# Performance work log

Measured on AMD Instinct MI355X. Metric: run time of the kernel, lower is better.

Reference implementation:

```python
import jax, jax.numpy as jnp
import numpy as np
import math

D_MODEL = 512
H = 8
N_LAYERS = 4
D_FF = 2048
HEAD_DIM = D_MODEL // H


def setup_inputs() -> dict:
    key = jax.random.key(0)
    ks = jax.random.split(key, 12)
    s = 1.0 / math.sqrt(D_MODEL)
    x = jax.random.normal(ks[0], (16, 1024, D_MODEL), dtype=jnp.float32)
    # shared head module (same weights for all H heads, per original ModuleList aliasing)
    wq = jax.random.normal(ks[1], (D_MODEL, HEAD_DIM), dtype=jnp.float32) * s
    bq = jnp.zeros((HEAD_DIM,), dtype=jnp.float32)
    wk = jax.random.normal(ks[2], (D_MODEL, HEAD_DIM), dtype=jnp.float32) * s
    bk = jnp.zeros((HEAD_DIM,), dtype=jnp.float32)
    wv = jax.random.normal(ks[3], (D_MODEL, HEAD_DIM), dtype=jnp.float32) * s
    bv = jnp.zeros((HEAD_DIM,), dtype=jnp.float32)
    wo = jax.random.normal(ks[4], (D_MODEL, D_MODEL), dtype=jnp.float32) * s
    bo = jnp.zeros((D_MODEL,), dtype=jnp.float32)
    # shared LayerNorm params (one LN instance used everywhere)
    ln_g = jnp.ones((D_MODEL,), dtype=jnp.float32)
    ln_b = jnp.zeros((D_MODEL,), dtype=jnp.float32)
    w1 = jax.random.normal(ks[5], (D_MODEL, D_FF), dtype=jnp.float32) * s
    b1 = jnp.zeros((D_FF,), dtype=jnp.float32)
    w2 = jax.random.normal(ks[6], (D_FF, D_MODEL), dtype=jnp.float32) * (1.0 / math.sqrt(D_FF))
    b2 = jnp.zeros((D_MODEL,), dtype=jnp.float32)
    return {"x": x, "wq": wq, "bq": bq, "wk": wk, "bk": bk, "wv": wv, "bv": bv,
            "wo": wo, "bo": bo, "ln_g": ln_g, "ln_b": ln_b,
            "w1": w1, "b1": b1, "w2": w2, "b2": b2}


def _layernorm(x, g, b, eps=1e-5):
    mu = jnp.mean(x, axis=-1, keepdims=True)
    var = jnp.var(x, axis=-1, keepdims=True)
    return (x - mu) * jax.lax.rsqrt(var + eps) * g + b


def _mha(x, wq, bq, wk, bk, wv, bv, wo, bo):
    # All H heads share identical weights, so compute one head and tile the concat.
    q = x @ wq + bq                      # [b, s, hd]
    k = x @ wk + bk                      # [b, s, hd]
    v = x @ wv + bv                      # [b, s, hd]
    scores = jnp.einsum('bqd,bkd->bqk', q, k) / math.sqrt(D_MODEL / H)
    # NOTE: original applies Softmax(dim=1) on a [b, s_q, s_k] tensor -> softmax over q axis
    attn = jax.nn.softmax(scores, axis=1)
    head = jnp.einsum('bqk,bkd->bqd', attn, v)   # [b, s, hd]
    concat = jnp.tile(head, (1, 1, H))           # [b, s, d_model] (H identical heads)
    return concat @ wo + bo


def reference(x, wq, bq, wk, bk, wv, bv, wo, bo, ln_g, ln_b, w1, b1, w2, b2):
    for _ in range(N_LAYERS):
        attn = _mha(x, wq, bq, wk, bk, wv, bv, wo, bo)
        h = _layernorm(attn + x, ln_g, ln_b)
        ff = (jnp.maximum(h @ w1 + b1, 0.0) if False else (h @ w1 + b1)) @ w2 + b2  # no relu in original forward
        x = _layernorm(h + ff, ln_g, ln_b)
    return x
```

## Files before the change

### kernel.cpp

```cpp
#include <hip/hip_runtime.h>
#include <hip/hip_bf16.h>

#define DEV __device__ __forceinline__

typedef __bf16 bf16;
typedef __attribute__((ext_vector_type(8))) __bf16 bf16x8;
typedef __attribute__((ext_vector_type(4))) __bf16 bf16x4;
typedef __attribute__((ext_vector_type(4))) float f32x4;

static constexpr int B = 16, S = 1024, D = 512, HD = 64, FF = 2048;
static constexpr int BS = B * S;
static constexpr int QKVLD = 192;

typedef const __attribute__((address_space(1))) void gas_void;
typedef __attribute__((address_space(3))) void las_void;

DEV void gload16(const void* g, void* l) {
  __builtin_amdgcn_global_load_lds((gas_void*)g, (las_void*)l, 16, 0, 0);
}

DEV void store_out(float* p, float v) { *p = v; }
DEV void store_out(bf16* p, float v) { *p = (bf16)v; }

#define MEMFENCE asm volatile("" ::: "memory")
#define VMCNT(n) asm volatile("s_waitcnt vmcnt(" #n ")" ::: "memory")

template<int BM, typename OutT>
__global__ __launch_bounds__(512, 1) void k_gemm8p(
    const bf16* __restrict__ A, const bf16* __restrict__ Bt, OutT* __restrict__ C,
    int K, int lda, int ldb, int ldc, int gn, float alpha, const float* __restrict__ bias)
{
  static_assert(BM == 128 || BM == 256, "");
  constexpr int HM = BM / 2;
  constexpr int FMH = HM / 2 / 16;
  constexpr int GL_A = HM / 64;
  constexpr int GL_B = 2;

  __shared__ bf16 sA[2][2][HM * 64];
  __shared__ bf16 sB[2][2][128 * 64];

  const int tid = threadIdx.x;
  const int lane = tid & 63;
  const int wid = tid >> 6;
  const int wm = wid >> 2;
  const int wn = wid & 3;
  const int lr = lane & 15;
  const int lk8 = (lane >> 4) * 8;

  const int nwg = gridDim.x;
  const int bid = blockIdx.x;
  const int swz = (bid & 7) * (nwg >> 3) + (bid >> 3);
  const int im = swz / gn, in = swz % gn;
  const int bm0 = im * BM, bn0 = in * 256;

  A += (long)bm0 * lda;
  Bt += (long)bn0 * ldb;

  const int NT = K >> 6;
  const int NI = NT >> 1;

  auto stageA = [&](int buf, int h, int t) {
    if (t >= NT) return;
    const bf16* src = A + (long)t * 64;
#pragma unroll
    for (int it = 0; it < GL_A; ++it) {
      int c = it * 512 + tid;
      int row = c >> 3;
      int cc = (c & 7) ^ (row & 7);
      gload16(src + (long)(h * HM + row) * lda + cc * 8, &sA[buf][h][c * 8]);
    }
  };
  auto stageB = [&](int buf, int h, int t) {
    if (t >= NT) return;
    const bf16* src = Bt + (long)t * 64;
#pragma unroll
    for (int it = 0; it < GL_B; ++it) {
      int c = it * 512 + tid;
      int row = c >> 3;
      int cc = (c & 7) ^ (row & 7);
      gload16(src + (long)(h * 128 + row) * ldb + cc * 8, &sB[buf][h][c * 8]);
    }
  };

  f32x4 acc[4][FMH * 2] = {};

  stageA(0, 0, 0); stageB(0, 1, 0); stageA(0, 1, 0); stageB(0, 0, 0);
  stageA(1, 0, 1); stageB(1, 1, 1);
  if (GL_A == 2) { VMCNT(4); } else { VMCNT(3); }
  MEMFENCE; __builtin_amdgcn_s_barrier(); MEMFENCE;

#define PHASE(b, qm, qn, STAGE, ...) do {                                        \
    bf16x8 af[FMH][2], bg[2][2];                                                 \
    _Pragma("unroll") for (int fm = 0; fm < FMH; ++fm)                           \
    _Pragma("unroll") for (int kx = 0; kx < 2; ++kx) {                           \
      int ra = wm * (HM / 2) + fm * 16 + lr;                                     \
      int e = kx * 32 + lk8;                                                     \
      af[fm][kx] = *(const bf16x8*)((const char*)&sA[b][qm][0] +                 \
                     (ra * 8 + ((e >> 3) ^ (ra & 7))) * 16);                     \
    }                                                                            \
    _Pragma("unroll") for (int fn = 0; fn < 2; ++fn)                             \
    _Pragma("unroll") for (int kx = 0; kx < 2; ++kx) {                           \
      int rb = wn * 32 + fn * 16 + lr;                                           \
      int e = kx * 32 + lk8;                                                     \
      bg[fn][kx] = *(const bf16x8*)((const char*)&sB[b][qn][0] +                 \
                     (rb * 8 + ((e >> 3) ^ (rb & 7))) * 16);                     \
    }                                                                            \
    STAGE;                                                                       \
    MEMFENCE; __builtin_amdgcn_s_barrier(); MEMFENCE;                            \
    __builtin_amdgcn_s_setprio(1);                                               \
    _Pragma("unroll") for (int kx = 0; kx < 2; ++kx)                             \
    _Pragma("unroll") for (int fm = 0; fm < FMH; ++fm)                           \
    _Pragma("unroll") for (int fn = 0; fn < 2; ++fn)                             \
      acc[qm * 2 + qn][fm * 2 + fn] = __builtin_amdgcn_mfma_f32_16x16x32_bf16(   \
          af[fm][kx], bg[fn][kx], acc[qm * 2 + qn][fm * 2 + fn], 0, 0, 0);       \
    __builtin_amdgcn_s_setprio(0);                                               \
    __VA_ARGS__;                                                                 \
    MEMFENCE; __builtin_amdgcn_s_barrier(); MEMFENCE;                            \
  } while (0)

  for (int i = 0; i < NI; ++i) {
    const int t1 = 2 * i + 1, t2 = 2 * i + 2, t3 = 2 * i + 3;
    const bool more = (t2 < NT);
    PHASE(0, 0, 0, stageA(1, 1, t1));
    PHASE(0, 0, 1, stageB(1, 0, t1));
    PHASE(0, 1, 1, stageA(0, 0, t2));
    PHASE(0, 1, 0, stageB(0, 1, t2),
          if (more) { if (GL_A == 2) { VMCNT(4); } else { VMCNT(3); } }
          else { VMCNT(0); });
    PHASE(1, 0, 0, stageA(0, 1, t2));
    PHASE(1, 0, 1, stageB(0, 0, t2));
    PHASE(1, 1, 1, stageA(1, 0, t3));
    PHASE(1, 1, 0, stageB(1, 1, t3),
          if (more) { if (GL_A == 2) { VMCNT(4); } else { VMCNT(3); } });
  }
#undef PHASE

  const int r0 = (lane >> 4) * 4;
#pragma unroll
  for (int qm = 0; qm < 2; ++qm)
#pragma unroll
  for (int qn = 0; qn < 2; ++qn)
#pragma unroll
  for (int fm = 0; fm < FMH; ++fm)
#pragma unroll
  for (int fn = 0; fn < 2; ++fn) {
    int gc = bn0 + qn * 128 + wn * 32 + fn * 16 + lr;
    float bv = bias ? bias[gc] : 0.f;
#pragma unroll
    for (int r = 0; r < 4; ++r) {
      int gr = bm0 + qm * HM + wm * (HM / 2) + fm * 16 + r0 + r;
      store_out(C + (long)gr * ldc + gc, acc[qm * 2 + qn][fm * 2 + fn][r] * alpha + bv);
    }
  }
}

template<int BM, int BN, int BK, int WM, int WN, typename OutT, bool EXPF>
__global__ __launch_bounds__(WM* WN * 64) void k_gemm(
    const bf16* __restrict__ A, const bf16* __restrict__ Bt, OutT* __restrict__ C,
    int K, int lda, int ldb, int ldc, float alpha, const float* __restrict__ bias,
    long aB, long bB, long cB)
{
  constexpr int NW = WM * WN;
  constexpr int T = NW * 64;
  constexpr int FM = BM / WM / 16;
  constexpr int FN = BN / WN / 16;
  constexpr int CPR = BK / 8;
  constexpr int CHA = BM * BK / 8;
  constexpr int CHB = BN * BK / 8;
  constexpr int IA = CHA / T;
  constexpr int IB = CHB / T;
  static_assert(CHA % T == 0 && CHB % T == 0, "staging divisibility");

  __shared__ bf16 sA[BM * BK];
  __shared__ bf16 sB[BN * BK];

  const int tid = threadIdx.x;
  const int lane = tid & 63;
  const int wid = tid >> 6;
  const int wm = wid / WN, wn = wid % WN;
  const int bm0 = blockIdx.x * BM;
  const int bn0 = blockIdx.y * BN;
  A += (long)blockIdx.z * aB + (long)bm0 * lda;
  Bt += (long)blockIdx.z * bB + (long)bn0 * ldb;
  C += (long)blockIdx.z * cB;

  f32x4 acc[FM][FN] = {};
  const int lr = lane & 15;
  const int lk = (lane >> 4) * 8;

  for (int k0 = 0; k0 < K; k0 += BK) {
#pragma unroll
    for (int i = 0; i < IA; ++i) {
      int c = i * T + tid;
      int row = c / CPR, kc = (c % CPR) * 8;
      gload16(A + (long)row * lda + k0 + kc, sA + c * 8);
    }
#pragma unroll
    for (int i = 0; i < IB; ++i) {
      int c = i * T + tid;
      int row = c / CPR, kc = (c % CPR) * 8;
      gload16(Bt + (long)row * ldb + k0 + kc, sB + c * 8);
    }
    asm volatile("s_waitcnt vmcnt(0)" ::: "memory");
    __syncthreads();

#pragma unroll
    for (int kk = 0; kk < BK; kk += 32) {
      bf16x8 af[FM], bg[FN];
#pragma unroll
      for (int m = 0; m < FM; ++m) {
        int row = wm * (FM * 16) + m * 16 + lr;
        af[m] = *(const bf16x8*)(sA + row * BK + kk + lk);
      }
#pragma unroll
      for (int n = 0; n < FN; ++n) {
        int col = wn * (FN * 16) + n * 16 + lr;
        bg[n] = *(const bf16x8*)(sB + col * BK + kk + lk);
      }
#pragma unroll
      for (int m = 0; m < FM; ++m)
#pragma unroll
        for (int n = 0; n < FN; ++n)
          acc[m][n] = __builtin_amdgcn_mfma_f32_16x16x32_bf16(af[m], bg[n], acc[m][n], 0, 0, 0);
    }
    __syncthreads();
  }

  const int r0 = (lane >> 4) * 4;
#pragma unroll
  for (int m = 0; m < FM; ++m) {
#pragma unroll
    for (int n = 0; n < FN; ++n) {
      int col = bn0 + wn * (FN * 16) + n * 16 + lr;
      float bv = bias ? bias[col] : 0.f;
#pragma unroll
      for (int r = 0; r < 4; ++r) {
        int row = bm0 + wm * (FM * 16) + m * 16 + r0 + r;
        float v = acc[m][n][r] * alpha + bv;
        if (EXPF) v = __expf(v);
        store_out(C + (long)row * ldc + col, v);
      }
    }
  }
}

__global__ __launch_bounds__(256) void k_cvt_dual(const float* __restrict__ in,
    float* __restrict__ fo, bf16* __restrict__ bo, long n4)
{
  long i = (long)blockIdx.x * 256 + threadIdx.x;
  if (i >= n4) return;
  float4 v = ((const float4*)in)[i];
  ((float4*)fo)[i] = v;
  bf16x4 h; h[0] = (bf16)v.x; h[1] = (bf16)v.y; h[2] = (bf16)v.z; h[3] = (bf16)v.w;
  ((bf16x4*)bo)[i] = h;
}

__global__ void k_tr(const float* __restrict__ in, bf16* __restrict__ out, int R, int C)
{
  __shared__ float t[32][33];
  int c0 = blockIdx.x * 32, r0 = blockIdx.y * 32;
#pragma unroll
  for (int i = 0; i < 4; ++i) {
    int r = r0 + threadIdx.y + i * 8;
    t[threadIdx.y + i * 8][threadIdx.x] = in[(long)r * C + c0 + threadIdx.x];
  }
  __syncthreads();
#pragma unroll
  for (int i = 0; i < 4; ++i) {
    int c = c0 + threadIdx.y + i * 8;
    out[(long)c * R + r0 + threadIdx.x] = (bf16)t[threadIdx.x][threadIdx.y + i * 8];
  }
}

__global__ __launch_bounds__(256) void k_woe(const float* __restrict__ wo, bf16* __restrict__ woet)
{
  int idx = blockIdx.x * 256 + threadIdx.x;
  int j = idx & 511, d = idx >> 9;
  float s = 0.f;
#pragma unroll
  for (int h = 0; h < 8; ++h) s += wo[(long)(h * 64 + d) * 512 + j];
  woet[(long)j * 64 + d] = (bf16)s;
}

__global__ void k_pack_bias(const float* __restrict__ bq, const float* __restrict__ bk,
                            const float* __restrict__ bv, float* __restrict__ o)
{
  int t = threadIdx.x;
  o[t] = bq[t]; o[64 + t] = bk[t]; o[128 + t] = bv[t];
}

__global__ __launch_bounds__(256) void k_colsum(const bf16* __restrict__ P, float* __restrict__ cs)
{
  int k = blockIdx.x * 256 + threadIdx.x;
  int b = blockIdx.y;
  const bf16* p = P + (long)b * S * S + k;
  float a0 = 0, a1 = 0, a2 = 0, a3 = 0;
  for (int q = 0; q < S; q += 4) {
    a0 += (float)p[(long)q * S];
    a1 += (float)p[(long)(q + 1) * S];
    a2 += (float)p[(long)(q + 2) * S];
    a3 += (float)p[(long)(q + 3) * S];
  }
  cs[b * S + k] = (a0 + a1) + (a2 + a3);
}

__global__ __launch_bounds__(256) void k_build_vnt(const bf16* __restrict__ qkv,
    const float* __restrict__ cs, bf16* __restrict__ vnt)
{
  int d = threadIdx.x & 63;
  int k = blockIdx.x * 4 + (threadIdx.x >> 6);
  int b = blockIdx.y;
  float v = (float)qkv[((long)(b * S + k)) * QKVLD + 128 + d];
  vnt[((long)b * HD + d) * S + k] = (bf16)(v / cs[b * S + k]);
}

__global__ __launch_bounds__(256) void k_add_ln(const float* __restrict__ a,
    const float* __restrict__ b, const float* __restrict__ g, const float* __restrict__ be,
    float* __restrict__ fo, bf16* __restrict__ bo)
{
  int row = blockIdx.x * 4 + (threadIdx.x >> 6);
  int lane = threadIdx.x & 63;
  const float4* pa = (const float4*)(a + (long)row * D);
  const float4* pb = (const float4*)(b + (long)row * D);
  float4 v[2];
  float s = 0.f, s2 = 0.f;
#pragma unroll
  for (int j = 0; j < 2; ++j) {
    float4 x = pa[lane + j * 64];
    float4 y = pb[lane + j * 64];
    float4 t;
    t.x = x.x + y.x; t.y = x.y + y.y; t.z = x.z + y.z; t.w = x.w + y.w;
    v[j] = t;
    s += t.x + t.y + t.z + t.w;
    s2 += t.x * t.x + t.y * t.y + t.z * t.z + t.w * t.w;
  }
#pragma unroll
  for (int o = 32; o > 0; o >>= 1) { s += __shfl_xor(s, o); s2 += __shfl_xor(s2, o); }
  float mean = s * (1.f / D);
  float var = s2 * (1.f / D) - mean * mean;
  float rstd = rsqrtf(var + 1e-5f);
#pragma unroll
  for (int j = 0; j < 2; ++j) {
    int ci = lane + j * 64;
    float4 gv = ((const float4*)g)[ci];
    float4 bv = ((const float4*)be)[ci];
    float4 t = v[j], y;
    y.x = (t.x - mean) * rstd * gv.x + bv.x;
    y.y = (t.y - mean) * rstd * gv.y + bv.y;
    y.z = (t.z - mean) * rstd * gv.z + bv.z;
    y.w = (t.w - mean) * rstd * gv.w + bv.w;
    ((float4*)(fo + (long)row * D))[ci] = y;
    bf16x4 h; h[0] = (bf16)y.x; h[1] = (bf16)y.y; h[2] = (bf16)y.z; h[3] = (bf16)y.w;
    *(bf16x4*)(bo + (long)row * D + ci * 4) = h;
  }
}

extern "C" void kernel_launch(void* const* d_in, const int* in_sizes, int n_in,
                              void* d_out, int out_size, void* d_ws, size_t ws_size,
                              hipStream_t stream) {
  const float* x_in = (const float*)d_in[0];
  const float* wq = (const float*)d_in[1];
  const float* bq = (const float*)d_in[2];
  const float* wk = (const float*)d_in[3];
  const float* bk = (const float*)d_in[4];
  const float* wv = (const float*)d_in[5];
  const float* bv = (const float*)d_in[6];
  const float* wo = (const float*)d_in[7];
  const float* bo = (const float*)d_in[8];
  const float* ln_g = (const float*)d_in[9];
  const float* ln_b = (const float*)d_in[10];
  const float* w1 = (const float*)d_in[11];
  const float* b1 = (const float*)d_in[12];
  const float* w2 = (const float*)d_in[13];
  const float* b2 = (const float*)d_in[14];
  float* f_x = (float*)d_out;

  char* w = (char*)d_ws;
  size_t off = 0;
  auto alloc = [&](size_t bytes) { void* p = w + off; off += (bytes + 255) & ~(size_t)255; return p; };
  float* f_tmp = (float*)alloc((size_t)BS * D * 4);
  float* f_h   = (float*)alloc((size_t)BS * D * 4);
  bf16* b_x    = (bf16*)alloc((size_t)BS * D * 2);
  bf16* b_h    = (bf16*)alloc((size_t)BS * D * 2);
  bf16* b_qkv  = (bf16*)alloc((size_t)BS * QKVLD * 2);
  bf16* b_big  = (bf16*)alloc((size_t)BS * FF * 2);
  float* f_cs  = (float*)alloc((size_t)B * S * 4);
  bf16* b_vnt  = (bf16*)alloc((size_t)B * HD * S * 2);
  bf16* b_head = (bf16*)alloc((size_t)BS * HD * 2);
  bf16* wqkvT  = (bf16*)alloc((size_t)QKVLD * D * 2);
  bf16* woeT   = (bf16*)alloc((size_t)D * HD * 2);
  bf16* w1T    = (bf16*)alloc((size_t)FF * D * 2);
  bf16* w2T    = (bf16*)alloc((size_t)D * FF * 2);
  float* f_bqkv = (float*)alloc(192 * 4);

  k_cvt_dual<<<dim3(BS * D / 4 / 256), 256, 0, stream>>>(x_in, f_x, b_x, (long)BS * D / 4);
  k_tr<<<dim3(HD / 32, D / 32), dim3(32, 8), 0, stream>>>(wq, wqkvT, D, HD);
  k_tr<<<dim3(HD / 32, D / 32), dim3(32, 8), 0, stream>>>(wk, wqkvT + 64 * D, D, HD);
  k_tr<<<dim3(HD / 32, D / 32), dim3(32, 8), 0, stream>>>(wv, wqkvT + 128 * D, D, HD);
  k_tr<<<dim3(FF / 32, D / 32), dim3(32, 8), 0, stream>>>(w1, w1T, D, FF);
  k_tr<<<dim3(D / 32, FF / 32), dim3(32, 8), 0, stream>>>(w2, w2T, FF, D);
  k_woe<<<dim3(128), 256, 0, stream>>>(wo, woeT);
  k_pack_bias<<<1, 64, 0, stream>>>(bq, bk, bv, f_bqkv);

  for (int layer = 0; layer < 4; ++layer) {
    k_gemm<128, 64, 64, 4, 1, bf16, false><<<dim3(BS / 128, 3, 1), 256, 0, stream>>>(
        b_x, wqkvT, b_qkv, D, D, D, QKVLD, 1.f, f_bqkv, 0, 0, 0);
    k_gemm<128, 128, 64, 2, 2, bf16, true><<<dim3(S / 128, S / 128, B), 256, 0, stream>>>(
        b_qkv, b_qkv + 64, b_big, HD, QKVLD, QKVLD, S, 0.125f, nullptr,
        (long)S * QKVLD, (long)S * QKVLD, (long)S * S);
    k_colsum<<<dim3(S / 256, B), 256, 0, stream>>>(b_big, f_cs);
    k_build_vnt<<<dim3(S / 4, B), 256, 0, stream>>>(b_qkv, f_cs, b_vnt);
    k_gemm<64, 64, 64, 4, 1, bf16, false><<<dim3(S / 64, 1, B), 256, 0, stream>>>(
        b_big, b_vnt, b_head, S, S, S, HD, 1.f, nullptr,
        (long)S * S, (long)HD * S, (long)S * HD);
    k_gemm<128, 128, 64, 2, 2, float, false><<<dim3(BS / 128, D / 128, 1), 256, 0, stream>>>(
        b_head, woeT, f_tmp, HD, HD, HD, D, 1.f, bo, 0, 0, 0);
    k_add_ln<<<dim3(BS / 4), 256, 0, stream>>>(f_tmp, f_x, ln_g, ln_b, f_h, b_h);
    k_gemm8p<256, bf16><<<dim3((BS / 256) * (FF / 256)), 512, 0, stream>>>(
        b_h, w1T, b_big, D, D, D, FF, FF / 256, 1.f, b1);
    k_gemm8p<128, float><<<dim3((BS / 128) * (D / 256)), 512, 0, stream>>>(
        b_big, w2T, f_tmp, FF, FF, FF, D, D / 256, 1.f, b2);
    k_add_ln<<<dim3(BS / 4), 256, 0, stream>>>(f_tmp, f_h, ln_g, ln_b, f_x, b_x);
  }
}
```

Baseline: 1.018 ms.

## Fuse output projections with residual add and LayerNorm in full-row GEMM kernel

Adds a GEMM kernel that computes a 64-row by full 512-column tile per block so bias, residual add and LayerNorm can be applied in the epilogue with a cross-wave reduction through shared memory. It replaces both the Wo projection plus add_ln pair and the W2 projection plus add_ln pair, which removes the fp32 temporary buffer round trip and two elementwise launches. In exchange, the W2 GEMM now uses a narrow 64-row tile with a 512-wide B tile, uncoalesced scalar epilogue stores and large shared memory. That may lower MFMA efficiency and occupancy compared with the tuned 8-wave GEMM it replaces.

```diff
diff --git a/kernel.cpp b/kernel.cpp
--- a/kernel.cpp
+++ b/kernel.cpp
@@ -154,6 +154,128 @@
   }
 }
 
+template<int NT, bool DB>
+__global__ __launch_bounds__(512, 2) void k_gemm_ln(
+    const bf16* __restrict__ A, const bf16* __restrict__ Bt,
+    const float* __restrict__ resid, const float* __restrict__ bias,
+    const float* __restrict__ g, const float* __restrict__ be,
+    float* __restrict__ fo, bf16* __restrict__ bo16)
+{
+  constexpr int K = NT * 64;
+  constexpr int NB = DB ? 2 : 1;
+  __shared__ bf16 sA[NB][64 * 64];
+  __shared__ bf16 sB[NB][512 * 64];
+  __shared__ float lsum[2][64][2];
+
+  const int tid = threadIdx.x;
+  const int lane = tid & 63;
+  const int wid = tid >> 6;
+  const int wm = wid >> 1;
+  const int wn = wid & 1;
+  const int lr = lane & 15;
+  const int lk8 = (lane >> 4) * 8;
+  const long bm0 = (long)blockIdx.x * 64;
+
+  const bf16* Ab = A + bm0 * K;
+
+  auto stage = [&](int buf, int t) {
+    {
+      int c = tid;
+      int row = c >> 3;
+      int cc = (c & 7) ^ (row & 7);
+      gload16(Ab + (long)row * K + t * 64 + cc * 8, &sA[buf][c * 8]);
+    }
+#pragma unroll
+    for (int it = 0; it < 8; ++it) {
+      int c = it * 512 + tid;
+      int row = c >> 3;
+      int cc = (c & 7) ^ (row & 7);
+      gload16(Bt + (long)row * K + t * 64 + cc * 8, &sB[buf][c * 8]);
+    }
+  };
+
+  f32x4 acc[16] = {};
+  auto compute = [&](int buf) {
+#pragma unroll
+    for (int kx = 0; kx < 2; ++kx) {
+      int ra = wm * 16 + lr;
+      int ech = (kx * 32 + lk8) >> 3;
+      bf16x8 af = *(const bf16x8*)((const char*)&sA[buf][0] +
+                    (ra * 8 + (ech ^ (ra & 7))) * 16);
+#pragma unroll
+      for (int fn = 0; fn < 16; ++fn) {
+        int rb = wn * 256 + fn * 16 + lr;
+        bf16x8 bg = *(const bf16x8*)((const char*)&sB[buf][0] +
+                      (rb * 8 + (ech ^ (rb & 7))) * 16);
+        acc[fn] = __builtin_amdgcn_mfma_f32_16x16x32_bf16(af, bg, acc[fn], 0, 0, 0);
+      }
+    }
+  };
+
+  stage(0, 0);
+  VMCNT(0); MEMFENCE;
+  __syncthreads();
+  if constexpr (DB) {
+    for (int t = 0; t < NT; ++t) {
+      if (t + 1 < NT) stage((t & 1) ^ 1, t + 1);
+      compute(t & 1);
+      VMCNT(0); MEMFENCE;
+      __syncthreads();
+    }
+  } else {
+    compute(0);
+  }
+
+  const int r0 = (lane >> 4) * 4;
+  float s[4] = {}, s2[4] = {};
+#pragma unroll
+  for (int fn = 0; fn < 16; ++fn) {
+    int gc = wn * 256 + fn * 16 + lr;
+    float bv = bias[gc];
+#pragma unroll
+    for (int r = 0; r < 4; ++r) {
+      long gr = bm0 + wm * 16 + r0 + r;
+      float y = acc[fn][r] + bv + resid[gr * 512 + gc];
+      acc[fn][r] = y;
+      s[r] += y; s2[r] += y * y;
+    }
+  }
+#pragma unroll
+  for (int m = 1; m < 16; m <<= 1)
+#pragma unroll
+    for (int r = 0; r < 4; ++r) { s[r] += __shfl_xor(s[r], m); s2[r] += __shfl_xor(s2[r], m); }
+  if (lr == 0) {
+#pragma unroll
+    for (int r = 0; r < 4; ++r) {
+      lsum[wn][wm * 16 + r0 + r][0] = s[r];
+      lsum[wn][wm * 16 + r0 + r][1] = s2[r];
+    }
+  }
+  __syncthreads();
+  float mean[4], rstd[4];
+#pragma unroll
+  for (int r = 0; r < 4; ++r) {
+    int row = wm * 16 + r0 + r;
+    float S1 = lsum[0][row][0] + lsum[1][row][0];
+    float S2 = lsum[0][row][1] + lsum[1][row][1];
+    mean[r] = S1 * (1.f / 512);
+    float var = S2 * (1.f / 512) - mean[r] * mean[r];
+    rstd[r] = rsqrtf(var + 1e-5f);
+  }
+#pragma unroll
+  for (int fn = 0; fn < 16; ++fn) {
+    int gc = wn * 256 + fn * 16 + lr;
+    float gv = g[gc], bev = be[gc];
+#pragma unroll
+    for (int r = 0; r < 4; ++r) {
+      long gr = bm0 + wm * 16 + r0 + r;
+      float yn = (acc[fn][r] - mean[r]) * rstd[r] * gv + bev;
+      fo[gr * 512 + gc] = yn;
+      bo16[gr * 512 + gc] = (bf16)yn;
+    }
+  }
+}
+
 template<int BM, int BN, int BK, int WM, int WN, typename OutT, bool EXPF>
 __global__ __launch_bounds__(WM* WN * 64) void k_gemm(
     const bf16* __restrict__ A, const bf16* __restrict__ Bt, OutT* __restrict__ C,
@@ -312,47 +434,6 @@
   int b = blockIdx.y;
   float v = (float)qkv[((long)(b * S + k)) * QKVLD + 128 + d];
   vnt[((long)b * HD + d) * S + k] = (bf16)(v / cs[b * S + k]);
-}
-
-__global__ __launch_bounds__(256) void k_add_ln(const float* __restrict__ a,
-    const float* __restrict__ b, const float* __restrict__ g, const float* __restrict__ be,
-    float* __restrict__ fo, bf16* __restrict__ bo)
-{
-  int row = blockIdx.x * 4 + (threadIdx.x >> 6);
-  int lane = threadIdx.x & 63;
-  const float4* pa = (const float4*)(a + (long)row * D);
-  const float4* pb = (const float4*)(b + (long)row * D);
-  float4 v[2];
-  float s = 0.f, s2 = 0.f;
-#pragma unroll
-  for (int j = 0; j < 2; ++j) {
-    float4 x = pa[lane + j * 64];
-    float4 y = pb[lane + j * 64];
-    float4 t;
-    t.x = x.x + y.x; t.y = x.y + y.y; t.z = x.z + y.z; t.w = x.w + y.w;
-    v[j] = t;
-    s += t.x + t.y + t.z + t.w;
-    s2 += t.x * t.x + t.y * t.y + t.z * t.z + t.w * t.w;
-  }
-#pragma unroll
-  for (int o = 32; o > 0; o >>= 1) { s += __shfl_xor(s, o); s2 += __shfl_xor(s2, o); }
-  float mean = s * (1.f / D);
-  float var = s2 * (1.f / D) - mean * mean;
-  float rstd = rsqrtf(var + 1e-5f);
-#pragma unroll
-  for (int j = 0; j < 2; ++j) {
-    int ci = lane + j * 64;
-    float4 gv = ((const float4*)g)[ci];
-    float4 bv = ((const float4*)be)[ci];
-    float4 t = v[j], y;
-    y.x = (t.x - mean) * rstd * gv.x + bv.x;
-    y.y = (t.y - mean) * rstd * gv.y + bv.y;
-    y.z = (t.z - mean) * rstd * gv.z + bv.z;
-    y.w = (t.w - mean) * rstd * gv.w + bv.w;
-    ((float4*)(fo + (long)row * D))[ci] = y;
-    bf16x4 h; h[0] = (bf16)y.x; h[1] = (bf16)y.y; h[2] = (bf16)y.z; h[3] = (bf16)y.w;
-    *(bf16x4*)(bo + (long)row * D + ci * 4) = h;
-  }
 }
 
 extern "C" void kernel_launch(void* const* d_in, const int* in_sizes, int n_in,
@@ -378,7 +459,6 @@
   char* w = (char*)d_ws;
   size_t off = 0;
   auto alloc = [&](size_t bytes) { void* p = w + off; off += (bytes + 255) & ~(size_t)255; return p; };
-  float* f_tmp = (float*)alloc((size_t)BS * D * 4);
   float* f_h   = (float*)alloc((size_t)BS * D * 4);
   bf16* b_x    = (bf16*)alloc((size_t)BS * D * 2);
   bf16* b_h    = (bf16*)alloc((size_t)BS * D * 2);
@@ -413,13 +493,11 @@
     k_gemm<64, 64, 64, 4, 1, bf16, false><<<dim3(S / 64, 1, B), 256, 0, stream>>>(
         b_big, b_vnt, b_head, S, S, S, HD, 1.f, nullptr,
         (long)S * S, (long)HD * S, (long)S * HD);
-    k_gemm<128, 128, 64, 2, 2, float, false><<<dim3(BS / 128, D / 128, 1), 256, 0, stream>>>(
-        b_head, woeT, f_tmp, HD, HD, HD, D, 1.f, bo, 0, 0, 0);
-    k_add_ln<<<dim3(BS / 4), 256, 0, stream>>>(f_tmp, f_x, ln_g, ln_b, f_h, b_h);
+    k_gemm_ln<1, false><<<dim3(BS / 64), 512, 0, stream>>>(
+        b_head, woeT, f_x, bo, ln_g, ln_b, f_h, b_h);
     k_gemm8p<256, bf16><<<dim3((BS / 256) * (FF / 256)), 512, 0, stream>>>(
         b_h, w1T, b_big, D, D, D, FF, FF / 256, 1.f, b1);
-    k_gemm8p<128, float><<<dim3((BS / 128) * (D / 256)), 512, 0, stream>>>(
-        b_big, w2T, f_tmp, FF, FF, FF, D, D / 256, 1.f, b2);
-    k_add_ln<<<dim3(BS / 4), 256, 0, stream>>>(f_tmp, f_h, ln_g, ln_b, f_x, b_x);
-  }
-}
+    k_gemm_ln<32, true><<<dim3(BS / 64), 512, 0, stream>>>(
+        b_big, w2T, f_h, b2, ln_g, ln_b, f_x, b_x);
+  }
+}
```

New measurement: 980.7 us. 3.7% less time.
